# Optimization experiments

Measured on AMD Instinct MI355X. Metric: run time of the kernel, lower is better.

Reference implementation:

```python
import jax, jax.numpy as jnp
import numpy as np

B, TED, G, N, E, MD, NOISE = 10000, 512, 64, 2000, 64000, 15, 128
PAC = 10
PACDIM = (TED + NOISE) * PAC  # 6400
D0, D1 = 1024, 512


def _linear_params(k, fan_in, fan_out):
    kw, kb = jax.random.split(k)
    lim = 1.0 / np.sqrt(fan_in)
    w = jax.random.uniform(kw, (fan_in, fan_out), minval=-lim, maxval=lim, dtype=jnp.float32)
    b = jax.random.uniform(kb, (fan_out,), minval=-lim, maxval=lim, dtype=jnp.float32)
    return w, b


def setup_inputs() -> dict:
    key = jax.random.key(0)
    ks = jax.random.split(key, 12)
    inp = {
        'input_': jax.random.normal(ks[0], (B, TED), dtype=jnp.float32),
        'graphs_x': jax.random.normal(ks[1], (G, N, 1), dtype=jnp.float32),
        'edge_index': jax.random.randint(ks[2], (G, 2, E), 0, N, dtype=jnp.int32),
        'graph_ids': jax.random.randint(ks[3], (B,), 0, G, dtype=jnp.int32),
        'chain': jax.random.normal(ks[4], (B, 1), dtype=jnp.float32),
        'metadata': jax.random.normal(ks[5], (B, MD), dtype=jnp.float32),
    }
    inp['gcn_w'], inp['gcn_b'] = _linear_params(ks[6], 1, 1)
    inp['meta_w'], inp['meta_b'] = _linear_params(ks[7], 1 + MD, 32)
    inp['gme_w'], inp['gme_b'] = _linear_params(ks[8], N + 32, NOISE)
    inp['seq_w0'], inp['seq_b0'] = _linear_params(ks[9], PACDIM, D0)
    inp['seq_w1'], inp['seq_b1'] = _linear_params(ks[10], D0, D1)
    inp['seq_w2'], inp['seq_b2'] = _linear_params(ks[11], D1, 1)
    return inp


def _gcn_one(x, ei, gcn_w, gcn_b):
    # GCNConv(1,1) with self-loops and symmetric normalization.
    loops = jnp.arange(N, dtype=ei.dtype)
    src = jnp.concatenate([ei[0], loops])
    dst = jnp.concatenate([ei[1], loops])
    deg = jax.ops.segment_sum(jnp.ones_like(src, dtype=x.dtype), dst, num_segments=N)
    dinv = jax.lax.rsqrt(deg)  # deg >= 1 due to self-loops
    norm = dinv[src] * dinv[dst]  # [E+N]
    xw = x @ gcn_w  # [N,1]
    msg = xw[src] * norm[:, None]
    out = jax.ops.segment_sum(msg, dst, num_segments=N) + gcn_b
    return out.reshape(-1)  # flatten -> [N]


def reference(input_, graphs_x, edge_index, graph_ids, chain, metadata,
              gcn_w, gcn_b, meta_w, meta_b, gme_w, gme_b,
              seq_w0, seq_b0, seq_w1, seq_b1, seq_w2, seq_b2):
    # per-unique-graph GCN, vectorized over G graphs
    gcn_out = jax.vmap(lambda x, ei: _gcn_one(x, ei, gcn_w, gcn_b))(graphs_x, edge_index)  # [G,N]
    graph_emb = gcn_out[graph_ids]  # gather: [B,N]
    all_meta = jnp.concatenate([chain, metadata], axis=1)  # [B,1+MD]
    meta_emb = jax.nn.relu(all_meta @ meta_w + meta_b)  # [B,32]
    noise = jnp.concatenate([graph_emb, meta_emb], axis=1) @ gme_w + gme_b  # [B,NOISE]
    h = jnp.concatenate([input_, noise], axis=1).reshape(-1, PACDIM)  # [B/PAC, PACDIM]
    h = jax.nn.leaky_relu(h @ seq_w0 + seq_b0, 0.2)  # dropout omitted (eval mode)
    h = jax.nn.leaky_relu(h @ seq_w1 + seq_b1, 0.2)
    return h @ seq_w2 + seq_b2  # [B/PAC, 1]
```

## Files before the change

kernel.cpp:

```cpp
#include <hip/hip_runtime.h>

typedef __bf16 bf16_t;
typedef __bf16 bf16x4 __attribute__((ext_vector_type(4)));
typedef __bf16 bf16x8 __attribute__((ext_vector_type(8)));
typedef float floatx4 __attribute__((ext_vector_type(4)));

#define G_GRAPHS 64
#define N_NODES 2000
#define N_EDGES 64000
#define BATCH 10000
#define TED_ 512
#define NOISE_ 128
#define PACDIM_ 6400
#define D0_ 1024
#define D1_ 512
#define MROWS 1000
#define ESPLIT 8
#define EPB (N_EDGES / ESPLIT)
#define S0 8
#define S1 8

__device__ __forceinline__ void glds16(const void* g, void* l) {
    __builtin_amdgcn_global_load_lds(
        (__attribute__((address_space(1))) void*)(g),
        (__attribute__((address_space(3))) void*)(l), 16, 0, 0);
}

__global__ __launch_bounds__(256) void prep_kernel(
    const int* __restrict__ edge_index, float* __restrict__ degs_part,
    const float* __restrict__ in, bf16_t* __restrict__ A,
    const float* __restrict__ W0, bf16_t* __restrict__ W0t,
    const float* __restrict__ W1, bf16_t* __restrict__ W1t)
{
    __shared__ float h[N_NODES];
    __shared__ float t[32][33];
    const int b = blockIdx.x, tid = threadIdx.x;
    if (b < 512) {
        const int s = b & 7, g = b >> 3;
        for (int n = tid; n < N_NODES; n += 256) h[n] = 0.f;
        __syncthreads();
        const int* dst = edge_index + (size_t)g * 2 * N_EDGES + N_EDGES + s * EPB;
        for (int e = tid; e < EPB; e += 256) atomicAdd(&h[dst[e]], 1.0f);
        __syncthreads();
        float* dp = degs_part + ((size_t)g * ESPLIT + s) * N_NODES;
        for (int n = tid; n < N_NODES; n += 256) dp[n] = h[n];
        return;
    }
    if (b < 5512) {
        int idx = (b - 512) * 256 + tid;
        float4 v = ((const float4*)in)[idx];
        int bb = idx >> 7;
        int c = (idx & 127) << 2;
        int r = bb / 10, slot = bb - r * 10;
        bf16x4 o = { (bf16_t)v.x, (bf16_t)v.y, (bf16_t)v.z, (bf16_t)v.w };
        *(bf16x4*)(A + (size_t)r * PACDIM_ + slot * 640 + c) = o;
        return;
    }
    const float* W; bf16_t* Wt; int Rr, Cc, c0, r0;
    if (b < 11912) {
        int tile = b - 5512;
        W = W0; Wt = W0t; Rr = PACDIM_; Cc = D0_;
        c0 = (tile & 31) << 5; r0 = (tile >> 5) << 5;
    } else {
        int tile = b - 11912;
        W = W1; Wt = W1t; Rr = D0_; Cc = D1_;
        c0 = (tile & 15) << 5; r0 = (tile >> 4) << 5;
    }
    int tx = tid & 31, ty = tid >> 5;
    for (int yy = ty; yy < 32; yy += 8)
        t[yy][tx] = W[(size_t)(r0 + yy) * Cc + c0 + tx];
    __syncthreads();
    for (int yy = ty; yy < 32; yy += 8)
        Wt[(size_t)(c0 + yy) * Rr + r0 + tx] = (bf16_t)t[tx][yy];
}

__global__ __launch_bounds__(512) void msg_kernel(
    const float* __restrict__ graphs_x, const int* __restrict__ edge_index,
    const float* __restrict__ degs_part, float* __restrict__ outs_part)
{
    __shared__ float xs[N_NODES];
    __shared__ float dv[N_NODES];
    __shared__ float oh[N_NODES];
    const int g = blockIdx.y, s = blockIdx.x, tid = threadIdx.x;
    const float* xg = graphs_x + (size_t)g * N_NODES;
    const float* dgp = degs_part + (size_t)g * ESPLIT * N_NODES;
    for (int n = tid; n < N_NODES; n += 512) {
        xs[n] = xg[n];
        float d = 1.0f;
        for (int p = 0; p < ESPLIT; p++) d += dgp[(size_t)p * N_NODES + n];
        dv[n] = rsqrtf(d);
        oh[n] = 0.f;
    }
    __syncthreads();
    const int* src = edge_index + (size_t)g * 2 * N_EDGES + s * EPB;
    const int* dst = src + N_EDGES;
    for (int e = tid; e < EPB; e += 512) {
        int ss = src[e], dd = dst[e];
        atomicAdd(&oh[dd], xs[ss] * dv[ss] * dv[dd]);
    }
    __syncthreads();
    float* op = outs_part + ((size_t)g * ESPLIT + s) * N_NODES;
    for (int n = tid; n < N_NODES; n += 512) op[n] = oh[n];
}

__global__ __launch_bounds__(512) void gnoise_kernel(
    const float* __restrict__ graphs_x, const float* __restrict__ degs_part,
    const float* __restrict__ outs_part,
    const float* __restrict__ gcn_w, const float* __restrict__ gcn_b,
    const float* __restrict__ gme_w, float* __restrict__ gnoise_p)
{
    __shared__ float of[500];
    __shared__ float part[4][128];
    const int s = blockIdx.x, g = blockIdx.y, tid = threadIdx.x;
    const int nBase = s * 500;
    const float w = gcn_w[0], bb = gcn_b[0];
    const float* dgp = degs_part + (size_t)g * ESPLIT * N_NODES;
    const float* otp = outs_part + (size_t)g * ESPLIT * N_NODES;
    for (int n = tid; n < 500; n += 512) {
        int gn = nBase + n;
        float d = 1.0f, o = 0.f;
        for (int p = 0; p < ESPLIT; p++) {
            d += dgp[(size_t)p * N_NODES + gn];
            o += otp[(size_t)p * N_NODES + gn];
        }
        of[n] = w * (o + graphs_x[(size_t)g * N_NODES + gn] / d) + bb;
    }
    __syncthreads();
    const int j = tid & 127, ch = tid >> 7;
    float acc = 0.f;
    const int n0 = ch * 125;
    for (int n = n0; n < n0 + 125; n++)
        acc += of[n] * gme_w[(size_t)(nBase + n) * 128 + j];
    part[ch][j] = acc;
    __syncthreads();
    if (tid < 128)
        gnoise_p[((size_t)g * 4 + s) * 128 + tid] =
            part[0][tid] + part[1][tid] + part[2][tid] + part[3][tid];
}

__global__ __launch_bounds__(256) void meta_kernel(
    const float* __restrict__ chain, const float* __restrict__ metadata,
    const int* __restrict__ graph_ids,
    const float* __restrict__ meta_w, const float* __restrict__ meta_b,
    const float* __restrict__ gme_w, const float* __restrict__ gme_b,
    const float* __restrict__ gnoise_p, bf16_t* __restrict__ A)
{
    int wid = (blockIdx.x * 256 + threadIdx.x) >> 6;
    int lane = threadIdx.x & 63;
    if (wid >= BATCH) return;
    const int b = wid;
    float me = 0.f;
    if (lane < 32) {
        me = meta_b[lane] + chain[b] * meta_w[lane];
        for (int i = 1; i < 16; i++)
            me += metadata[(size_t)b * 15 + (i - 1)] * meta_w[(size_t)i * 32 + lane];
        me = me > 0.f ? me : 0.f;
    }
    const int gid = graph_ids[b];
    const float* gp = gnoise_p + (size_t)gid * 4 * 128;
    const int j1 = lane, j2 = lane + 64;
    float n1 = gme_b[j1] + gp[j1] + gp[128 + j1] + gp[256 + j1] + gp[384 + j1];
    float n2 = gme_b[j2] + gp[j2] + gp[128 + j2] + gp[256 + j2] + gp[384 + j2];
    for (int k = 0; k < 32; k++) {
        float mk = __shfl(me, k, 64);
        const float* wrow = gme_w + (size_t)(N_NODES + k) * 128;
        n1 += mk * wrow[j1];
        n2 += mk * wrow[j2];
    }
    int r = b / 10, slot = b - r * 10;
    bf16_t* dp = A + (size_t)r * PACDIM_ + slot * 640 + TED_;
    dp[j1] = (bf16_t)n1;
    dp[j2] = (bf16_t)n2;
}

__global__ __launch_bounds__(256) void gemm_bt_splitk_kernel(
    const bf16_t* __restrict__ A,
    const bf16_t* __restrict__ Bt,
    float* __restrict__ P,
    int M, int N, int K, int KS)
{
    __shared__ __align__(16) bf16_t As[2][128 * 32];
    __shared__ __align__(16) bf16_t Bs[2][128 * 32];
    const int tid = threadIdx.x;
    const int wave = tid >> 6;
    const int lane = tid & 63;
    const int mBase = blockIdx.y * 128;
    const int nBase = blockIdx.x * 128;
    const int z = blockIdx.z;
    const int Mp = gridDim.y * 128;
    const int wm = (wave & 1) * 64;
    const int wn = (wave >> 1) * 64;

    floatx4 acc[4][4] = {};

    const int rA0 = tid >> 2, k80 = (tid & 3) * 8;
    int gm0 = mBase + rA0;      if (gm0 > M - 1) gm0 = M - 1;
    int gm1 = mBase + 64 + rA0; if (gm1 > M - 1) gm1 = M - 1;
    const bf16_t* aP0 = A + (size_t)gm0 * K + k80;
    const bf16_t* aP1 = A + (size_t)gm1 * K + k80;
    const bf16_t* bP0 = Bt + (size_t)(nBase + rA0) * K + k80;
    const bf16_t* bP1 = Bt + (size_t)(nBase + 64 + rA0) * K + k80;

    const int kq = (lane >> 4) * 8;
    const int mr = lane & 15;
    int aOff[4], bOff[4];
    for (int i = 0; i < 4; i++) aOff[i] = (wm + i * 16 + mr) * 32 + kq;
    for (int j = 0; j < 4; j++) bOff[j] = (wn + j * 16 + mr) * 32 + kq;

    const int nIter = KS >> 5;
    const int kc = z * KS;
    {
        char* lA = (char*)(&As[0][0]) + wave * 1024;
        char* lB = (char*)(&Bs[0][0]) + wave * 1024;
        glds16(aP0 + kc, lA);
        glds16(aP1 + kc, lA + 4096);
        glds16(bP0 + kc, lB);
        glds16(bP1 + kc, lB + 4096);
    }
    __syncthreads();
    for (int t = 0; t < nIter; ++t) {
        const int cur = t & 1;
        if (t + 1 < nIter) {
            const int kn = kc + (t + 1) * 32;
            char* lA = (char*)(&As[cur ^ 1][0]) + wave * 1024;
            char* lB = (char*)(&Bs[cur ^ 1][0]) + wave * 1024;
            glds16(aP0 + kn, lA);
            glds16(aP1 + kn, lA + 4096);
            glds16(bP0 + kn, lB);
            glds16(bP1 + kn, lB + 4096);
        }
        const bf16_t* aB = &As[cur][0];
        const bf16_t* bB = &Bs[cur][0];
        bf16x8 af[4], bfr[4];
        for (int i = 0; i < 4; i++) af[i] = *(const bf16x8*)(aB + aOff[i]);
        for (int j = 0; j < 4; j++) bfr[j] = *(const bf16x8*)(bB + bOff[j]);
        for (int i = 0; i < 4; i++)
            for (int j = 0; j < 4; j++)
                acc[i][j] = __builtin_amdgcn_mfma_f32_16x16x32_bf16(
                    af[i], bfr[j], acc[i][j], 0, 0, 0);
        __syncthreads();
    }

    float* Pz = P + (size_t)z * Mp * N;
    const int rq = (lane >> 4) * 4;
    const int cn = lane & 15;
    for (int j = 0; j < 4; j++) {
        int col = nBase + wn + j * 16 + cn;
        for (int i = 0; i < 4; i++)
            for (int r = 0; r < 4; r++) {
                int rowm = mBase + wm + i * 16 + rq + r;
                Pz[(size_t)rowm * N + col] = acc[i][j][r];
            }
    }
}

__global__ __launch_bounds__(256) void reduce_bias_leaky_kernel(
    const float* __restrict__ P, const float* __restrict__ bias,
    bf16_t* __restrict__ C, int M, int N, int Mp, int S)
{
    int idx = blockIdx.x * 256 + threadIdx.x;
    int total = M * (N >> 2);
    if (idx >= total) return;
    int nv = N >> 2;
    int r = idx / nv, c4 = (idx - r * nv) << 2;
    size_t off = (size_t)r * N + c4;
    size_t stride = (size_t)Mp * N;
    float4 v = *(const float4*)(P + off);
    for (int s = 1; s < S; s++) {
        float4 u = *(const float4*)(P + s * stride + off);
        v.x += u.x; v.y += u.y; v.z += u.z; v.w += u.w;
    }
    const float4 bv = *(const float4*)(bias + c4);
    v.x += bv.x; v.y += bv.y; v.z += bv.z; v.w += bv.w;
    v.x = v.x > 0.f ? v.x : 0.2f * v.x;
    v.y = v.y > 0.f ? v.y : 0.2f * v.y;
    v.z = v.z > 0.f ? v.z : 0.2f * v.z;
    v.w = v.w > 0.f ? v.w : 0.2f * v.w;
    bf16x4 o = { (bf16_t)v.x, (bf16_t)v.y, (bf16_t)v.z, (bf16_t)v.w };
    *(bf16x4*)(C + off) = o;
}

__global__ __launch_bounds__(256) void final_fused_kernel(
    const float* __restrict__ P, const float* __restrict__ b1,
    const float* __restrict__ w2, const float* __restrict__ b2,
    float* __restrict__ out, int Mp, int S)
{
    int wid = (blockIdx.x * 256 + threadIdx.x) >> 6;
    int lane = threadIdx.x & 63;
    if (wid >= MROWS) return;
    size_t stride = (size_t)Mp * D1_;
    const float* base = P + (size_t)wid * D1_;
    float s = 0.f;
    for (int i = 0; i < 8; i++) {
        int c = i * 64 + lane;
        float v = base[c];
        for (int z = 1; z < S; z++) v += base[(size_t)z * stride + c];
        v += b1[c];
        v = v > 0.f ? v : 0.2f * v;
        s += v * w2[c];
    }
    for (int off = 32; off; off >>= 1) s += __shfl_down(s, off, 64);
    if (lane == 0) out[wid] = s + b2[0];
}

extern "C" void kernel_launch(void* const* d_in, const int* in_sizes, int n_in,
                              void* d_out, int out_size, void* d_ws, size_t ws_size,
                              hipStream_t stream)
{
    const float* input_    = (const float*)d_in[0];
    const float* graphs_x  = (const float*)d_in[1];
    const int*   edge_idx  = (const int*)  d_in[2];
    const int*   graph_ids = (const int*)  d_in[3];
    const float* chain     = (const float*)d_in[4];
    const float* metadata  = (const float*)d_in[5];
    const float* gcn_w     = (const float*)d_in[6];
    const float* gcn_b     = (const float*)d_in[7];
    const float* meta_w    = (const float*)d_in[8];
    const float* meta_b    = (const float*)d_in[9];
    const float* gme_w     = (const float*)d_in[10];
    const float* gme_b     = (const float*)d_in[11];
    const float* seq_w0    = (const float*)d_in[12];
    const float* seq_b0    = (const float*)d_in[13];
    const float* seq_w1    = (const float*)d_in[14];
    const float* seq_b1    = (const float*)d_in[15];
    const float* seq_w2    = (const float*)d_in[16];
    const float* seq_b2    = (const float*)d_in[17];
    float* out = (float*)d_out;

    char* ws = (char*)d_ws;
    float*  degs_part = (float*)(ws + 0);
    float*  outs_part = (float*)(ws + 4096000);
    float*  gnoise_p  = (float*)(ws + 8192000);
    bf16_t* Abuf      = (bf16_t*)(ws + 8323072);
    bf16_t* W0t       = (bf16_t*)(ws + 21123072);
    bf16_t* W1t       = (bf16_t*)(ws + 34230272);
    bf16_t* H1        = (bf16_t*)(ws + 35278848);
    float*  P         = (float*)(ws + 37326848);

    prep_kernel<<<12424, 256, 0, stream>>>(
        edge_idx, degs_part, input_, Abuf, seq_w0, W0t, seq_w1, W1t);
    msg_kernel<<<dim3(ESPLIT, G_GRAPHS), 512, 0, stream>>>(
        graphs_x, edge_idx, degs_part, outs_part);
    gnoise_kernel<<<dim3(4, G_GRAPHS), 512, 0, stream>>>(
        graphs_x, degs_part, outs_part, gcn_w, gcn_b, gme_w, gnoise_p);
    meta_kernel<<<2500, 256, 0, stream>>>(
        chain, metadata, graph_ids, meta_w, meta_b, gme_w, gme_b,
        gnoise_p, Abuf);

    gemm_bt_splitk_kernel<<<dim3(D0_ / 128, 8, S0), 256, 0, stream>>>(
        Abuf, W0t, P, MROWS, D0_, PACDIM_, PACDIM_ / S0);
    reduce_bias_leaky_kernel<<<(MROWS * D0_ / 4 + 255) / 256, 256, 0, stream>>>(
        P, seq_b0, H1, MROWS, D0_, 1024, S0);

    gemm_bt_splitk_kernel<<<dim3(D1_ / 128, 8, S1), 256, 0, stream>>>(
        H1, W1t, P, MROWS, D1_, D0_, D0_ / S1);
    final_fused_kernel<<<(MROWS * 64 + 255) / 256, 256, 0, stream>>>(
        P, seq_b1, seq_w2, seq_b2, out, 1024, S1);
}
```

Before: 266.2 us.

## Fuse per-graph GCN and noise projection into prep kernel; remap GEMM block ids

Folds the degree count, message passing and graph-noise projection into single per-graph blocks inside the prep kernel, dropping two kernel launches and the partial-sum buffers. The GEMM kernel now takes a 1D grid and decodes split-k, N-tile and M-tile from the block id with split-k innermost, which changes how blocks are ordered across CUs for L2 reuse. The trade-off is that each graph is handled by one 256-thread block doing 64k edges twice serially, so the graph path may become a long tail inside the prep kernel.

```diff
diff --git a/kernel.cpp b/kernel.cpp
--- a/kernel.cpp
+++ b/kernel.cpp
@@ -15,10 +15,13 @@
 #define D0_ 1024
 #define D1_ 512
 #define MROWS 1000
-#define ESPLIT 8
-#define EPB (N_EDGES / ESPLIT)
 #define S0 8
 #define S1 8
+
+#define GRAPH_BLKS 64
+#define PACK_BLKS 5000
+#define W0T_BLKS 6400
+#define W1T_BLKS 512
 
 __device__ __forceinline__ void glds16(const void* g, void* l) {
     __builtin_amdgcn_global_load_lds(
@@ -27,27 +30,58 @@
 }
 
 __global__ __launch_bounds__(256) void prep_kernel(
-    const int* __restrict__ edge_index, float* __restrict__ degs_part,
+    const int* __restrict__ edge_index, const float* __restrict__ graphs_x,
+    const float* __restrict__ gcn_w, const float* __restrict__ gcn_b,
+    const float* __restrict__ gme_w, const float* __restrict__ gme_b,
+    float* __restrict__ gnoise,
     const float* __restrict__ in, bf16_t* __restrict__ A,
     const float* __restrict__ W0, bf16_t* __restrict__ W0t,
     const float* __restrict__ W1, bf16_t* __restrict__ W1t)
 {
-    __shared__ float h[N_NODES];
-    __shared__ float t[32][33];
+    __shared__ __align__(16) char smraw[25088];
     const int b = blockIdx.x, tid = threadIdx.x;
-    if (b < 512) {
-        const int s = b & 7, g = b >> 3;
-        for (int n = tid; n < N_NODES; n += 256) h[n] = 0.f;
-        __syncthreads();
-        const int* dst = edge_index + (size_t)g * 2 * N_EDGES + N_EDGES + s * EPB;
-        for (int e = tid; e < EPB; e += 256) atomicAdd(&h[dst[e]], 1.0f);
-        __syncthreads();
-        float* dp = degs_part + ((size_t)g * ESPLIT + s) * N_NODES;
-        for (int n = tid; n < N_NODES; n += 256) dp[n] = h[n];
+
+    if (b < GRAPH_BLKS) {
+        float* xs = (float*)smraw;
+        float* dg = xs + N_NODES;
+        float* oh = dg + N_NODES;
+        float* part = oh + N_NODES;
+        const int g = b;
+        const float* xg = graphs_x + (size_t)g * N_NODES;
+        for (int n = tid; n < N_NODES; n += 256) {
+            xs[n] = xg[n]; dg[n] = 0.f; oh[n] = 0.f;
+        }
+        __syncthreads();
+        const int* src = edge_index + (size_t)g * 2 * N_EDGES;
+        const int* dst = src + N_EDGES;
+        for (int e = tid; e < N_EDGES; e += 256) atomicAdd(&dg[dst[e]], 1.0f);
+        __syncthreads();
+        for (int n = tid; n < N_NODES; n += 256) dg[n] = rsqrtf(dg[n] + 1.0f);
+        __syncthreads();
+        for (int e = tid; e < N_EDGES; e += 256) {
+            int ss = src[e], dd = dst[e];
+            atomicAdd(&oh[dd], xs[ss] * dg[ss] * dg[dd]);
+        }
+        __syncthreads();
+        const float w = gcn_w[0], bb = gcn_b[0];
+        for (int n = tid; n < N_NODES; n += 256)
+            oh[n] = w * (oh[n] + xs[n] * dg[n] * dg[n]) + bb;
+        __syncthreads();
+        const int j = tid & 127, ch = tid >> 7;
+        const float* wp = gme_w + (size_t)(ch * 1000) * 128 + j;
+        const float* op = oh + ch * 1000;
+        float acc = 0.f;
+        #pragma unroll 4
+        for (int n = 0; n < 1000; n++)
+            acc += op[n] * wp[(size_t)n * 128];
+        part[ch * 128 + j] = acc;
+        __syncthreads();
+        if (tid < 128)
+            gnoise[(size_t)g * 128 + tid] = part[tid] + part[128 + tid] + gme_b[tid];
         return;
     }
-    if (b < 5512) {
-        int idx = (b - 512) * 256 + tid;
+    if (b < GRAPH_BLKS + PACK_BLKS) {
+        int idx = (b - GRAPH_BLKS) * 256 + tid;
         float4 v = ((const float4*)in)[idx];
         int bb = idx >> 7;
         int c = (idx & 127) << 2;
@@ -56,13 +90,14 @@
         *(bf16x4*)(A + (size_t)r * PACDIM_ + slot * 640 + c) = o;
         return;
     }
+    float (*t)[33] = (float(*)[33])smraw;
     const float* W; bf16_t* Wt; int Rr, Cc, c0, r0;
-    if (b < 11912) {
-        int tile = b - 5512;
+    if (b < GRAPH_BLKS + PACK_BLKS + W0T_BLKS) {
+        int tile = b - (GRAPH_BLKS + PACK_BLKS);
         W = W0; Wt = W0t; Rr = PACDIM_; Cc = D0_;
         c0 = (tile & 31) << 5; r0 = (tile >> 5) << 5;
     } else {
-        int tile = b - 11912;
+        int tile = b - (GRAPH_BLKS + PACK_BLKS + W0T_BLKS);
         W = W1; Wt = W1t; Rr = D0_; Cc = D1_;
         c0 = (tile & 15) << 5; r0 = (tile >> 4) << 5;
     }
@@ -74,76 +109,12 @@
         Wt[(size_t)(c0 + yy) * Rr + r0 + tx] = (bf16_t)t[tx][yy];
 }
 
-__global__ __launch_bounds__(512) void msg_kernel(
-    const float* __restrict__ graphs_x, const int* __restrict__ edge_index,
-    const float* __restrict__ degs_part, float* __restrict__ outs_part)
-{
-    __shared__ float xs[N_NODES];
-    __shared__ float dv[N_NODES];
-    __shared__ float oh[N_NODES];
-    const int g = blockIdx.y, s = blockIdx.x, tid = threadIdx.x;
-    const float* xg = graphs_x + (size_t)g * N_NODES;
-    const float* dgp = degs_part + (size_t)g * ESPLIT * N_NODES;
-    for (int n = tid; n < N_NODES; n += 512) {
-        xs[n] = xg[n];
-        float d = 1.0f;
-        for (int p = 0; p < ESPLIT; p++) d += dgp[(size_t)p * N_NODES + n];
-        dv[n] = rsqrtf(d);
-        oh[n] = 0.f;
-    }
-    __syncthreads();
-    const int* src = edge_index + (size_t)g * 2 * N_EDGES + s * EPB;
-    const int* dst = src + N_EDGES;
-    for (int e = tid; e < EPB; e += 512) {
-        int ss = src[e], dd = dst[e];
-        atomicAdd(&oh[dd], xs[ss] * dv[ss] * dv[dd]);
-    }
-    __syncthreads();
-    float* op = outs_part + ((size_t)g * ESPLIT + s) * N_NODES;
-    for (int n = tid; n < N_NODES; n += 512) op[n] = oh[n];
-}
-
-__global__ __launch_bounds__(512) void gnoise_kernel(
-    const float* __restrict__ graphs_x, const float* __restrict__ degs_part,
-    const float* __restrict__ outs_part,
-    const float* __restrict__ gcn_w, const float* __restrict__ gcn_b,
-    const float* __restrict__ gme_w, float* __restrict__ gnoise_p)
-{
-    __shared__ float of[500];
-    __shared__ float part[4][128];
-    const int s = blockIdx.x, g = blockIdx.y, tid = threadIdx.x;
-    const int nBase = s * 500;
-    const float w = gcn_w[0], bb = gcn_b[0];
-    const float* dgp = degs_part + (size_t)g * ESPLIT * N_NODES;
-    const float* otp = outs_part + (size_t)g * ESPLIT * N_NODES;
-    for (int n = tid; n < 500; n += 512) {
-        int gn = nBase + n;
-        float d = 1.0f, o = 0.f;
-        for (int p = 0; p < ESPLIT; p++) {
-            d += dgp[(size_t)p * N_NODES + gn];
-            o += otp[(size_t)p * N_NODES + gn];
-        }
-        of[n] = w * (o + graphs_x[(size_t)g * N_NODES + gn] / d) + bb;
-    }
-    __syncthreads();
-    const int j = tid & 127, ch = tid >> 7;
-    float acc = 0.f;
-    const int n0 = ch * 125;
-    for (int n = n0; n < n0 + 125; n++)
-        acc += of[n] * gme_w[(size_t)(nBase + n) * 128 + j];
-    part[ch][j] = acc;
-    __syncthreads();
-    if (tid < 128)
-        gnoise_p[((size_t)g * 4 + s) * 128 + tid] =
-            part[0][tid] + part[1][tid] + part[2][tid] + part[3][tid];
-}
-
 __global__ __launch_bounds__(256) void meta_kernel(
     const float* __restrict__ chain, const float* __restrict__ metadata,
     const int* __restrict__ graph_ids,
     const float* __restrict__ meta_w, const float* __restrict__ meta_b,
-    const float* __restrict__ gme_w, const float* __restrict__ gme_b,
-    const float* __restrict__ gnoise_p, bf16_t* __restrict__ A)
+    const float* __restrict__ gme_w,
+    const float* __restrict__ gnoise, bf16_t* __restrict__ A)
 {
     int wid = (blockIdx.x * 256 + threadIdx.x) >> 6;
     int lane = threadIdx.x & 63;
@@ -157,10 +128,10 @@
         me = me > 0.f ? me : 0.f;
     }
     const int gid = graph_ids[b];
-    const float* gp = gnoise_p + (size_t)gid * 4 * 128;
+    const float* gp = gnoise + (size_t)gid * 128;
     const int j1 = lane, j2 = lane + 64;
-    float n1 = gme_b[j1] + gp[j1] + gp[128 + j1] + gp[256 + j1] + gp[384 + j1];
-    float n2 = gme_b[j2] + gp[j2] + gp[128 + j2] + gp[256 + j2] + gp[384 + j2];
+    float n1 = gp[j1];
+    float n2 = gp[j2];
     for (int k = 0; k < 32; k++) {
         float mk = __shfl(me, k, 64);
         const float* wrow = gme_w + (size_t)(N_NODES + k) * 128;
@@ -177,17 +148,19 @@
     const bf16_t* __restrict__ A,
     const bf16_t* __restrict__ Bt,
     float* __restrict__ P,
-    int M, int N, int K, int KS)
+    int M, int N, int K, int KS, int zbits, int xbits, int Mp)
 {
     __shared__ __align__(16) bf16_t As[2][128 * 32];
     __shared__ __align__(16) bf16_t Bs[2][128 * 32];
     const int tid = threadIdx.x;
     const int wave = tid >> 6;
     const int lane = tid & 63;
-    const int mBase = blockIdx.y * 128;
-    const int nBase = blockIdx.x * 128;
-    const int z = blockIdx.z;
-    const int Mp = gridDim.y * 128;
+    const int id = blockIdx.x;
+    const int z = id & ((1 << zbits) - 1);
+    const int xt = (id >> zbits) & ((1 << xbits) - 1);
+    const int yt = id >> (zbits + xbits);
+    const int mBase = yt * 128;
+    const int nBase = xt * 128;
     const int wm = (wave & 1) * 64;
     const int wn = (wave >> 1) * 64;
 
@@ -328,32 +301,26 @@
     float* out = (float*)d_out;
 
     char* ws = (char*)d_ws;
-    float*  degs_part = (float*)(ws + 0);
-    float*  outs_part = (float*)(ws + 4096000);
-    float*  gnoise_p  = (float*)(ws + 8192000);
-    bf16_t* Abuf      = (bf16_t*)(ws + 8323072);
-    bf16_t* W0t       = (bf16_t*)(ws + 21123072);
-    bf16_t* W1t       = (bf16_t*)(ws + 34230272);
-    bf16_t* H1        = (bf16_t*)(ws + 35278848);
-    float*  P         = (float*)(ws + 37326848);
-
-    prep_kernel<<<12424, 256, 0, stream>>>(
-        edge_idx, degs_part, input_, Abuf, seq_w0, W0t, seq_w1, W1t);
-    msg_kernel<<<dim3(ESPLIT, G_GRAPHS), 512, 0, stream>>>(
-        graphs_x, edge_idx, degs_part, outs_part);
-    gnoise_kernel<<<dim3(4, G_GRAPHS), 512, 0, stream>>>(
-        graphs_x, degs_part, outs_part, gcn_w, gcn_b, gme_w, gnoise_p);
+    float*  gnoise = (float*)(ws + 0);
+    bf16_t* Abuf   = (bf16_t*)(ws + 32768);
+    bf16_t* W0t    = (bf16_t*)(ws + 12832768);
+    bf16_t* W1t    = (bf16_t*)(ws + 25939968);
+    bf16_t* H1     = (bf16_t*)(ws + 26988544);
+    float*  P      = (float*)(ws + 29036544);
+
+    prep_kernel<<<GRAPH_BLKS + PACK_BLKS + W0T_BLKS + W1T_BLKS, 256, 0, stream>>>(
+        edge_idx, graphs_x, gcn_w, gcn_b, gme_w, gme_b, gnoise,
+        input_, Abuf, seq_w0, W0t, seq_w1, W1t);
     meta_kernel<<<2500, 256, 0, stream>>>(
-        chain, metadata, graph_ids, meta_w, meta_b, gme_w, gme_b,
-        gnoise_p, Abuf);
-
-    gemm_bt_splitk_kernel<<<dim3(D0_ / 128, 8, S0), 256, 0, stream>>>(
-        Abuf, W0t, P, MROWS, D0_, PACDIM_, PACDIM_ / S0);
+        chain, metadata, graph_ids, meta_w, meta_b, gme_w, gnoise, Abuf);
+
+    gemm_bt_splitk_kernel<<<512, 256, 0, stream>>>(
+        Abuf, W0t, P, MROWS, D0_, PACDIM_, PACDIM_ / S0, 3, 3, 1024);
     reduce_bias_leaky_kernel<<<(MROWS * D0_ / 4 + 255) / 256, 256, 0, stream>>>(
         P, seq_b0, H1, MROWS, D0_, 1024, S0);
 
-    gemm_bt_splitk_kernel<<<dim3(D1_ / 128, 8, S1), 256, 0, stream>>>(
-        H1, W1t, P, MROWS, D1_, D0_, D0_ / S1);
+    gemm_bt_splitk_kernel<<<256, 256, 0, stream>>>(
+        H1, W1t, P, MROWS, D1_, D0_, D0_ / S1, 3, 2, 1024);
     final_fused_kernel<<<(MROWS * 64 + 255) / 256, 256, 0, stream>>>(
         P, seq_b1, seq_w2, seq_b2, out, 1024, S1);
 }
```

Result: slower. 462.8 us (+73.9%).
